# Kernel optimization log

Hardware: AMD Instinct MI355X
Metric: run time of the kernel (lower is better)

The kernel has to match this reference:

```python
import jax, jax.numpy as jnp
import numpy as np

V, D, H, B, S, K = 10000, 128, 512, 32, 512, 2  # vocab, emb, hidden, batch, seq, num_cells

def setup_inputs() -> dict:
    key = jax.random.key(0)
    ks = jax.random.split(key, 8)
    sc_d, sc_h = 1.0 / np.sqrt(D), 1.0 / np.sqrt(H)
    return {
        "x": jax.random.randint(ks[0], (B, S), 0, V),
        "emb_table": jax.random.normal(ks[1], (V, D), jnp.float32),
        "W_ih": jax.random.uniform(ks[2], (K, 4 * H, D), jnp.float32, -sc_d, sc_d),
        "W_hh": jax.random.uniform(ks[3], (K, 4 * H, H), jnp.float32, -sc_h, sc_h),
        "b_ih": jax.random.uniform(ks[4], (K, 4 * H), jnp.float32, -sc_h, sc_h),
        "b_hh": jax.random.uniform(ks[5], (K, 4 * H), jnp.float32, -sc_h, sc_h),
        "W_out": jax.random.uniform(ks[6], (V, H), jnp.float32, -sc_h, sc_h),
        "b_out": jax.random.uniform(ks[7], (V,), jnp.float32, -sc_h, sc_h),
    }

def _mlstm(x_ids_t, emb_t, W_ih, W_hh, b, h0, c0):
    # x_ids_t: (S,B) int, emb_t: (S,B,D). Two LSTMCells; token id parity picks the cell.
    def step(carry, inp):
        h, c = carry                       # (B,H) each
        xt, ids = inp                      # (B,D), (B,)
        gates = (jnp.einsum('bd,kgd->kbg', xt, W_ih)
                 + jnp.einsum('bh,kgh->kbg', h, W_hh)
                 + b[:, None, :])          # (K,B,4H)
        i, f, g, o = jnp.split(gates, 4, axis=-1)
        i, f, o = jax.nn.sigmoid(i), jax.nn.sigmoid(f), jax.nn.sigmoid(o)
        g = jnp.tanh(g)
        c_new = f * c + i * g              # (K,B,H)
        h_new = o * jnp.tanh(c_new)        # (K,B,H)
        sel = (ids % 2)[:, None]           # (B,1) cell index per example
        h_next = jnp.where(sel == 0, h_new[0], h_new[1])
        c_next = jnp.where(sel == 0, c_new[0], c_new[1])
        return (h_next, c_next), h_next
    (_, _), hs = jax.lax.scan(step, (h0, c0), (emb_t, x_ids_t))
    return hs  # (S,B,H)

def reference(x, emb_table, W_ih, W_hh, b_ih, b_hh, W_out, b_out):
    emb = emb_table[x]                     # (B,S,D)
    emb_t = jnp.transpose(emb, (1, 0, 2))  # (S,B,D) time-major
    h0 = jnp.zeros((x.shape[0], W_hh.shape[-1]), emb.dtype)
    hs = _mlstm(x.T, emb_t, W_ih, W_hh, b_ih + b_hh, h0, h0)  # (S,B,H)
    flat = hs.reshape(-1, hs.shape[-1])    # (S*B, H)
    logits = flat @ W_out.T + b_out        # (S*B, V)
    return jax.nn.log_softmax(logits, axis=1)
```

## Files before the change

### kernel.cpp

```cpp
#include <hip/hip_runtime.h>
#include <hip/hip_bf16.h>

typedef __attribute__((ext_vector_type(8))) short short8;
typedef __attribute__((ext_vector_type(4))) float f32x4;
typedef unsigned long long u64;

#define V_N 10000
#define D_E 128
#define H_N 512
#define B_N 32
#define S_N 512

#define SENT64 0xFFFFFFFFFFFFFFFFull

#define OFF_RP    0
#define OFF_EMB   5242880
#define OFF_HS    (OFF_EMB + 4194304)
#define OFF_WOUT  (OFF_HS + 16777216)

__device__ __forceinline__ float ftanh(float x) {
  float e = __expf(-2.f * fabsf(x));
  float r = (1.f - e) / (1.f + e);
  return __builtin_copysignf(r, x);
}

union U128 { f32x4 f; u64 q[2]; };

__global__ void k_prep_emb(const int* __restrict__ x, const float* __restrict__ tab,
                           __hip_bfloat16* __restrict__ emb) {
  int i = blockIdx.x * 256 + threadIdx.x;
  if (i >= S_N * B_N * D_E) return;
  int d  = i & (D_E - 1);
  int sb = i >> 7;
  int b  = sb & (B_N - 1);
  int s  = sb >> 5;
  int tok = x[b * S_N + s];
  emb[i] = __float2bfloat16(tab[tok * D_E + d]);
}

__global__ void k_prep_wout(const float* __restrict__ w, __hip_bfloat16* __restrict__ o) {
  int i = blockIdx.x * 256 + threadIdx.x;
  if (i < V_N * H_N) o[i] = __float2bfloat16(w[i]);
}

__launch_bounds__(256, 1)
__global__ void k_recurrence(const int* __restrict__ x,
                             const float* __restrict__ W_ih, const float* __restrict__ W_hh,
                             const float* __restrict__ b_ih, const float* __restrict__ b_hh,
                             const __hip_bfloat16* __restrict__ emb,
                             __hip_bfloat16* __restrict__ hs)
{
  __shared__ __align__(16) __hip_bfloat16 Bl[32][648];
  __shared__ float gl4[4][64][33];
  __shared__ float bias[64];
  __shared__ unsigned short hloc[8][32];

  const int tid = threadIdx.x;
  const int wg  = blockIdx.x;
  const int lane = tid & 63, kw = tid >> 6;
  const int lrow = lane & 15, lk = (lane >> 4) * 8;
  const int b_ep = tid & 31, jj_ep = tid >> 5;

  short8 Afrag[20];
  #pragma unroll
  for (int mt = 0; mt < 4; ++mt) {
    #pragma unroll
    for (int ks = 0; ks < 5; ++ks) {
      int lr = mt * 16 + lrow;
      int q = lr >> 4, kc = (lr >> 3) & 1, jj = lr & 7;
      int grow = kc * 2048 + q * 512 + wg * 8 + jj;
      int c0 = kw * 160 + ks * 32 + lk;
      short8 a;
      #pragma unroll
      for (int e = 0; e < 8; ++e) {
        int c = c0 + e;
        float v = (c < 128) ? W_ih[(size_t)grow * 128 + c]
                            : W_hh[(size_t)grow * 512 + (c - 128)];
        __hip_bfloat16 hb = __float2bfloat16(v);
        a[e] = *(const short*)&hb;
      }
      Afrag[mt * 5 + ks] = a;
    }
  }
  if (tid < 64) {
    int lr = tid;
    int q = lr >> 4, kc = (lr >> 3) & 1, jj = lr & 7;
    int grow = kc * 2048 + q * 512 + wg * 8 + jj;
    bias[lr] = b_ih[grow] + b_hh[grow];
  }

  unsigned par[16];
  #pragma unroll
  for (int w = 0; w < 16; ++w) {
    unsigned p = 0;
    for (int bb = 0; bb < 32; ++bb)
      p |= (unsigned)(x[b_ep * S_N + w * 32 + bb] & 1) << bb;
    par[w] = p;
  }

  float c_state = 0.f;

  for (int t = 0; t < S_N; ++t) {
    {
      const f32x4* e16 = (const f32x4*)(emb + (size_t)t * B_N * D_E);
      #pragma unroll
      for (int c = 0; c < 2; ++c) {
        int ci = c * 256 + tid;
        int ex = ci >> 4, col = ci & 15;
        *(f32x4*)((char*)&Bl[0][0] + ex * 1296 + col * 16) = e16[ci];
      }
    }
    if (t == 0) {
      for (int i = tid; i < 4096; i += 256) {
        int b = i >> 7, hh = i & 127;
        *(u64*)&Bl[b][128 + hh * 4] = 0ull;
      }
    } else {
      const char* srcb = (const char*)hs + (size_t)(t - 1) * 32768;
      U128 buf[8];
      unsigned pend = 0xFFu;
      while (pend) {
        #pragma unroll
        for (int c = 0; c < 8; ++c)
          if (pend & (1u << c))
            asm volatile("global_load_dwordx4 %0, %1, off sc0 sc1"
                         : "=v"(buf[c].f) : "v"(srcb + (c * 4096 + tid * 16)) : "memory");
        asm volatile("s_waitcnt vmcnt(0)" ::: "memory");
        __builtin_amdgcn_sched_barrier(0);
        #pragma unroll
        for (int c = 0; c < 8; ++c)
          if ((pend & (1u << c)) && buf[c].q[0] != SENT64 && buf[c].q[1] != SENT64) {
            int ci = c * 256 + tid;
            *(f32x4*)((char*)&Bl[0][0] + (ci >> 6) * 1296 + 256 + (ci & 63) * 16) = buf[c].f;
            pend &= ~(1u << c);
          }
      }
    }
    __syncthreads();

    {
      f32x4 acc[4][2] = {};
      #pragma unroll
      for (int ks = 0; ks < 5; ++ks) {
        int cb = (kw * 160 + ks * 32 + lk) * 2;
        short8 b0 = *(const short8*)((const char*)&Bl[0][0] + lrow * 1296 + cb);
        short8 b1 = *(const short8*)((const char*)&Bl[0][0] + (16 + lrow) * 1296 + cb);
        #pragma unroll
        for (int mt = 0; mt < 4; ++mt) {
          acc[mt][0] = __builtin_amdgcn_mfma_f32_16x16x32_bf16(Afrag[mt * 5 + ks], b0, acc[mt][0], 0, 0, 0);
          acc[mt][1] = __builtin_amdgcn_mfma_f32_16x16x32_bf16(Afrag[mt * 5 + ks], b1, acc[mt][1], 0, 0, 0);
        }
      }
      #pragma unroll
      for (int mt = 0; mt < 4; ++mt)
        #pragma unroll
        for (int nt = 0; nt < 2; ++nt)
          #pragma unroll
          for (int r = 0; r < 4; ++r)
            gl4[kw][mt * 16 + (lane >> 4) * 4 + r][nt * 16 + (lane & 15)] = acc[mt][nt][r];
    }
    __syncthreads();

    {
      float cand_c[2], cand_h[2];
      #pragma unroll
      for (int k = 0; k < 2; ++k) {
        int base = k * 8 + jj_ep;
        float ig = gl4[0][base][b_ep] + gl4[1][base][b_ep]
                 + gl4[2][base][b_ep] + gl4[3][base][b_ep] + bias[base];
        float fg = gl4[0][16 + base][b_ep] + gl4[1][16 + base][b_ep]
                 + gl4[2][16 + base][b_ep] + gl4[3][16 + base][b_ep] + bias[16 + base];
        float gg = gl4[0][32 + base][b_ep] + gl4[1][32 + base][b_ep]
                 + gl4[2][32 + base][b_ep] + gl4[3][32 + base][b_ep] + bias[32 + base];
        float og = gl4[0][48 + base][b_ep] + gl4[1][48 + base][b_ep]
                 + gl4[2][48 + base][b_ep] + gl4[3][48 + base][b_ep] + bias[48 + base];
        ig = 1.f / (1.f + __expf(-ig));
        fg = 1.f / (1.f + __expf(-fg));
        og = 1.f / (1.f + __expf(-og));
        gg = ftanh(gg);
        float cn = fg * c_state + ig * gg;
        cand_c[k] = cn;
        cand_h[k] = og * ftanh(cn);
      }
      int sel = (par[t >> 5] >> (t & 31)) & 1;
      c_state  = sel ? cand_c[1] : cand_c[0];
      float hv = sel ? cand_h[1] : cand_h[0];
      __hip_bfloat16 hb = __float2bfloat16(hv);
      hloc[jj_ep][b_ep] = *(const unsigned short*)&hb;
    }
    __syncthreads();

    if (tid < 64) {
      int b = tid >> 1, half = tid & 1;
      u64 v = (u64)hloc[half * 4 + 0][b]
            | ((u64)hloc[half * 4 + 1][b] << 16)
            | ((u64)hloc[half * 4 + 2][b] << 32)
            | ((u64)hloc[half * 4 + 3][b] << 48);
      u64* dst = (u64*)hs + (size_t)t * 4096 + b * 128 + wg * 2 + half;
      __hip_atomic_store(dst, v, __ATOMIC_RELAXED, __HIP_MEMORY_SCOPE_AGENT);
    }
  }
}

__launch_bounds__(256, 2)
__global__ void k_gemm(const __hip_bfloat16* __restrict__ hs,
                       const __hip_bfloat16* __restrict__ wout,
                       const float* __restrict__ b_out,
                       float* __restrict__ out,
                       float* __restrict__ rowpart)
{
  __shared__ __hip_bfloat16 Al[128][72];
  __shared__ __hip_bfloat16 Wt[128][72];
  __shared__ float sumLDS[2][128];
  const int tid = threadIdx.x;
  const int tn = blockIdx.x, tm = blockIdx.y;
  const int lane = tid & 63, wv = tid >> 6;
  const int mq = wv & 1, nq = wv >> 1;
  const int lrow = lane & 15, lk = (lane >> 4) * 8;
  f32x4 acc[4][4] = {};

  const int ar = tid >> 3, ac = (tid & 7) * 8;
  for (int k0 = 0; k0 < 512; k0 += 64) {
    __syncthreads();
    #pragma unroll
    for (int rr = 0; rr < 4; ++rr) {
      int r = ar + rr * 32;
      short8 av = *(const short8*)(hs + ((size_t)(tm * 128 + r)) * 512 + k0 + ac);
      *(short8*)&Al[r][ac] = av;
      int v = tn * 128 + r;
      short8 wvv = {};
      if (v < V_N) wvv = *(const short8*)(wout + (size_t)v * 512 + k0 + ac);
      *(short8*)&Wt[r][ac] = wvv;
    }
    __syncthreads();
    #pragma unroll
    for (int ks = 0; ks < 2; ++ks) {
      int kb = ks * 32 + lk;
      short8 af[4], bf[4];
      #pragma unroll
      for (int i = 0; i < 4; ++i) af[i] = *(const short8*)&Al[mq * 64 + i * 16 + lrow][kb];
      #pragma unroll
      for (int i = 0; i < 4; ++i) bf[i] = *(const short8*)&Wt[nq * 64 + i * 16 + lrow][kb];
      #pragma unroll
      for (int i = 0; i < 4; ++i)
        #pragma unroll
        for (int jx = 0; jx < 4; ++jx)
          acc[i][jx] = __builtin_amdgcn_mfma_f32_16x16x32_bf16(af[i], bf[jx], acc[i][jx], 0, 0, 0);
    }
  }
  const int rbase = tm * 128 + mq * 64 + (lane >> 4) * 4;
  const int cbase = tn * 128 + nq * 64 + (lane & 15);
  float esum[4][4];
  #pragma unroll
  for (int i = 0; i < 4; ++i)
    #pragma unroll
    for (int r = 0; r < 4; ++r) esum[i][r] = 0.f;

  #pragma unroll
  for (int i = 0; i < 4; ++i) {
    #pragma unroll
    for (int jx = 0; jx < 4; ++jx) {
      int col = cbase + jx * 16;
      if (col < V_N) {
        float bo = b_out[col];
        #pragma unroll
        for (int r = 0; r < 4; ++r) {
          int row = rbase + i * 16 + r;
          float lg = acc[i][jx][r] + bo;
          out[(size_t)row * V_N + col] = lg;
          esum[i][r] += __expf(lg);
        }
      }
    }
  }
  #pragma unroll
  for (int i = 0; i < 4; ++i) {
    #pragma unroll
    for (int r = 0; r < 4; ++r) {
      float s = esum[i][r];
      s += __shfl_xor(s, 1); s += __shfl_xor(s, 2);
      s += __shfl_xor(s, 4); s += __shfl_xor(s, 8);
      if ((lane & 15) == 0)
        sumLDS[nq][mq * 64 + i * 16 + (lane >> 4) * 4 + r] = s;
    }
  }
  __syncthreads();
  if (tid < 128)
    rowpart[(size_t)(tm * 128 + tid) * 80 + tn] = sumLDS[0][tid] + sumLDS[1][tid];
}

__launch_bounds__(256)
__global__ void k_lsm_fix(float* __restrict__ out, const float* __restrict__ rowpart) {
  const int r = blockIdx.x;
  const float* rp = rowpart + (size_t)r * 80;
  float s = 0.f;
  for (int p = 0; p < 79; ++p) s += rp[p];
  float lse = __logf(s);
  float4* q4 = (float4*)(out + (size_t)r * V_N);
  for (int i = threadIdx.x; i < V_N / 4; i += 256) {
    float4 v = q4[i];
    v.x -= lse; v.y -= lse; v.z -= lse; v.w -= lse;
    q4[i] = v;
  }
}

extern "C" void kernel_launch(void* const* d_in, const int* in_sizes, int n_in,
                              void* d_out, int out_size, void* d_ws, size_t ws_size,
                              hipStream_t stream) {
  const int*   x    = (const int*)d_in[0];
  const float* tab  = (const float*)d_in[1];
  const float* Wih  = (const float*)d_in[2];
  const float* Whh  = (const float*)d_in[3];
  const float* bih  = (const float*)d_in[4];
  const float* bhh  = (const float*)d_in[5];
  const float* Wout = (const float*)d_in[6];
  const float* bout = (const float*)d_in[7];
  float* out = (float*)d_out;

  char* ws = (char*)d_ws;
  float*           rowpart = (float*)(ws + OFF_RP);
  __hip_bfloat16*  emb     = (__hip_bfloat16*)(ws + OFF_EMB);
  __hip_bfloat16*  hsbuf   = (__hip_bfloat16*)(ws + OFF_HS);
  __hip_bfloat16*  wob     = (__hip_bfloat16*)(ws + OFF_WOUT);

  hipMemsetAsync(hsbuf, 0xFF, (size_t)S_N * B_N * H_N * 2, stream);
  k_prep_emb<<<(S_N * B_N * D_E) / 256, 256, 0, stream>>>(x, tab, emb);
  k_prep_wout<<<(V_N * H_N) / 256, 256, 0, stream>>>(Wout, wob);
  k_recurrence<<<64, 256, 0, stream>>>(x, Wih, Whh, bih, bhh, emb, hsbuf);
  k_gemm<<<dim3(79, 128), 256, 0, stream>>>(hsbuf, wob, bout, out, rowpart);
  k_lsm_fix<<<16384, 256, 0, stream>>>(out, rowpart);
}
```

Baseline: 2.556 ms.

## Repartition LSTM recurrence into 16 workgroups of 1024 threads

Measured after the change: 4.535 ms. 1.77x slower.

```diff
diff --git a/kernel.cpp b/kernel.cpp
--- a/kernel.cpp
+++ b/kernel.cpp
@@ -43,7 +43,7 @@
   if (i < V_N * H_N) o[i] = __float2bfloat16(w[i]);
 }
 
-__launch_bounds__(256, 1)
+__launch_bounds__(1024, 1)
 __global__ void k_recurrence(const int* __restrict__ x,
                              const float* __restrict__ W_ih, const float* __restrict__ W_hh,
                              const float* __restrict__ b_ih, const float* __restrict__ b_hh,
@@ -51,25 +51,26 @@
                              __hip_bfloat16* __restrict__ hs)
 {
   __shared__ __align__(16) __hip_bfloat16 Bl[32][648];
-  __shared__ float gl4[4][64][33];
-  __shared__ float bias[64];
-  __shared__ unsigned short hloc[8][32];
+  __shared__ float gl[2][256][33];
+  __shared__ float bias[256];
+  __shared__ unsigned short hloc[32][32];
 
   const int tid = threadIdx.x;
   const int wg  = blockIdx.x;
-  const int lane = tid & 63, kw = tid >> 6;
+  const int lane = tid & 63, wv = tid >> 6;
+  const int rg  = wv >> 1, ks2 = wv & 1;
   const int lrow = lane & 15, lk = (lane >> 4) * 8;
   const int b_ep = tid & 31, jj_ep = tid >> 5;
 
   short8 Afrag[20];
   #pragma unroll
-  for (int mt = 0; mt < 4; ++mt) {
-    #pragma unroll
-    for (int ks = 0; ks < 5; ++ks) {
-      int lr = mt * 16 + lrow;
-      int q = lr >> 4, kc = (lr >> 3) & 1, jj = lr & 7;
-      int grow = kc * 2048 + q * 512 + wg * 8 + jj;
-      int c0 = kw * 160 + ks * 32 + lk;
+  for (int mt = 0; mt < 2; ++mt) {
+    #pragma unroll
+    for (int ks = 0; ks < 10; ++ks) {
+      int lr = rg * 32 + mt * 16 + lrow;
+      int q = lr >> 6, kc = (lr >> 5) & 1, jj = lr & 31;
+      int grow = kc * 2048 + q * 512 + wg * 32 + jj;
+      int c0 = ks2 * 320 + ks * 32 + lk;
       short8 a;
       #pragma unroll
       for (int e = 0; e < 8; ++e) {
@@ -79,13 +80,13 @@
         __hip_bfloat16 hb = __float2bfloat16(v);
         a[e] = *(const short*)&hb;
       }
-      Afrag[mt * 5 + ks] = a;
-    }
-  }
-  if (tid < 64) {
+      Afrag[mt * 10 + ks] = a;
+    }
+  }
+  if (tid < 256) {
     int lr = tid;
-    int q = lr >> 4, kc = (lr >> 3) & 1, jj = lr & 7;
-    int grow = kc * 2048 + q * 512 + wg * 8 + jj;
+    int q = lr >> 6, kc = (lr >> 5) & 1, jj = lr & 31;
+    int grow = kc * 2048 + q * 512 + wg * 32 + jj;
     bias[lr] = b_ih[grow] + b_hh[grow];
   }
 
@@ -101,36 +102,32 @@
   float c_state = 0.f;
 
   for (int t = 0; t < S_N; ++t) {
-    {
+    if (tid < 512) {
       const f32x4* e16 = (const f32x4*)(emb + (size_t)t * B_N * D_E);
-      #pragma unroll
-      for (int c = 0; c < 2; ++c) {
-        int ci = c * 256 + tid;
-        int ex = ci >> 4, col = ci & 15;
-        *(f32x4*)((char*)&Bl[0][0] + ex * 1296 + col * 16) = e16[ci];
-      }
+      int ex = tid >> 4, col = tid & 15;
+      *(f32x4*)((char*)&Bl[0][0] + ex * 1296 + col * 16) = e16[tid];
     }
     if (t == 0) {
-      for (int i = tid; i < 4096; i += 256) {
+      for (int i = tid; i < 4096; i += 1024) {
         int b = i >> 7, hh = i & 127;
         *(u64*)&Bl[b][128 + hh * 4] = 0ull;
       }
     } else {
       const char* srcb = (const char*)hs + (size_t)(t - 1) * 32768;
-      U128 buf[8];
-      unsigned pend = 0xFFu;
+      U128 buf[2];
+      unsigned pend = 3u;
       while (pend) {
         #pragma unroll
-        for (int c = 0; c < 8; ++c)
+        for (int c = 0; c < 2; ++c)
           if (pend & (1u << c))
             asm volatile("global_load_dwordx4 %0, %1, off sc0 sc1"
-                         : "=v"(buf[c].f) : "v"(srcb + (c * 4096 + tid * 16)) : "memory");
+                         : "=v"(buf[c].f) : "v"(srcb + (c * 16384 + tid * 16)) : "memory");
         asm volatile("s_waitcnt vmcnt(0)" ::: "memory");
         __builtin_amdgcn_sched_barrier(0);
         #pragma unroll
-        for (int c = 0; c < 8; ++c)
+        for (int c = 0; c < 2; ++c)
           if ((pend & (1u << c)) && buf[c].q[0] != SENT64 && buf[c].q[1] != SENT64) {
-            int ci = c * 256 + tid;
+            int ci = c * 1024 + tid;
             *(f32x4*)((char*)&Bl[0][0] + (ci >> 6) * 1296 + 256 + (ci & 63) * 16) = buf[c].f;
             pend &= ~(1u << c);
           }
@@ -139,48 +136,44 @@
     __syncthreads();
 
     {
-      f32x4 acc[4][2] = {};
-      #pragma unroll
-      for (int ks = 0; ks < 5; ++ks) {
-        int cb = (kw * 160 + ks * 32 + lk) * 2;
+      f32x4 acc[2][2] = {};
+      #pragma unroll
+      for (int ks = 0; ks < 10; ++ks) {
+        int cb = (ks2 * 320 + ks * 32 + lk) * 2;
         short8 b0 = *(const short8*)((const char*)&Bl[0][0] + lrow * 1296 + cb);
         short8 b1 = *(const short8*)((const char*)&Bl[0][0] + (16 + lrow) * 1296 + cb);
         #pragma unroll
-        for (int mt = 0; mt < 4; ++mt) {
-          acc[mt][0] = __builtin_amdgcn_mfma_f32_16x16x32_bf16(Afrag[mt * 5 + ks], b0, acc[mt][0], 0, 0, 0);
-          acc[mt][1] = __builtin_amdgcn_mfma_f32_16x16x32_bf16(Afrag[mt * 5 + ks], b1, acc[mt][1], 0, 0, 0);
+        for (int mt = 0; mt < 2; ++mt) {
+          acc[mt][0] = __builtin_amdgcn_mfma_f32_16x16x32_bf16(Afrag[mt * 10 + ks], b0, acc[mt][0], 0, 0, 0);
+          acc[mt][1] = __builtin_amdgcn_mfma_f32_16x16x32_bf16(Afrag[mt * 10 + ks], b1, acc[mt][1], 0, 0, 0);
         }
       }
       #pragma unroll
-      for (int mt = 0; mt < 4; ++mt)
+      for (int mt = 0; mt < 2; ++mt)
         #pragma unroll
         for (int nt = 0; nt < 2; ++nt)
           #pragma unroll
           for (int r = 0; r < 4; ++r)
-            gl4[kw][mt * 16 + (lane >> 4) * 4 + r][nt * 16 + (lane & 15)] = acc[mt][nt][r];
+            gl[ks2][rg * 32 + mt * 16 + (lane >> 4) * 4 + r][nt * 16 + (lane & 15)] = acc[mt][nt][r];
     }
     __syncthreads();
 
     {
       float cand_c[2], cand_h[2];
       #pragma unroll
-      for (int k = 0; k < 2; ++k) {
-        int base = k * 8 + jj_ep;
-        float ig = gl4[0][base][b_ep] + gl4[1][base][b_ep]
-                 + gl4[2][base][b_ep] + gl4[3][base][b_ep] + bias[base];
-        float fg = gl4[0][16 + base][b_ep] + gl4[1][16 + base][b_ep]
-                 + gl4[2][16 + base][b_ep] + gl4[3][16 + base][b_ep] + bias[16 + base];
-        float gg = gl4[0][32 + base][b_ep] + gl4[1][32 + base][b_ep]
-                 + gl4[2][32 + base][b_ep] + gl4[3][32 + base][b_ep] + bias[32 + base];
-        float og = gl4[0][48 + base][b_ep] + gl4[1][48 + base][b_ep]
-                 + gl4[2][48 + base][b_ep] + gl4[3][48 + base][b_ep] + bias[48 + base];
+      for (int kc = 0; kc < 2; ++kc) {
+        int base = kc * 32 + jj_ep;
+        float ig = gl[0][base][b_ep]       + gl[1][base][b_ep]       + bias[base];
+        float fg = gl[0][64 + base][b_ep]  + gl[1][64 + base][b_ep]  + bias[64 + base];
+        float gg = gl[0][128 + base][b_ep] + gl[1][128 + base][b_ep] + bias[128 + base];
+        float og = gl[0][192 + base][b_ep] + gl[1][192 + base][b_ep] + bias[192 + base];
         ig = 1.f / (1.f + __expf(-ig));
         fg = 1.f / (1.f + __expf(-fg));
         og = 1.f / (1.f + __expf(-og));
         gg = ftanh(gg);
         float cn = fg * c_state + ig * gg;
-        cand_c[k] = cn;
-        cand_h[k] = og * ftanh(cn);
+        cand_c[kc] = cn;
+        cand_h[kc] = og * ftanh(cn);
       }
       int sel = (par[t >> 5] >> (t & 31)) & 1;
       c_state  = sel ? cand_c[1] : cand_c[0];
@@ -190,13 +183,13 @@
     }
     __syncthreads();
 
-    if (tid < 64) {
-      int b = tid >> 1, half = tid & 1;
-      u64 v = (u64)hloc[half * 4 + 0][b]
-            | ((u64)hloc[half * 4 + 1][b] << 16)
-            | ((u64)hloc[half * 4 + 2][b] << 32)
-            | ((u64)hloc[half * 4 + 3][b] << 48);
-      u64* dst = (u64*)hs + (size_t)t * 4096 + b * 128 + wg * 2 + half;
+    if (tid < 256) {
+      int ex = tid >> 3, part = tid & 7;
+      u64 v = (u64)hloc[part * 4 + 0][ex]
+            | ((u64)hloc[part * 4 + 1][ex] << 16)
+            | ((u64)hloc[part * 4 + 2][ex] << 32)
+            | ((u64)hloc[part * 4 + 3][ex] << 48);
+      u64* dst = (u64*)hs + (size_t)t * 4096 + ex * 128 + wg * 8 + part;
       __hip_atomic_store(dst, v, __ATOMIC_RELAXED, __HIP_MEMORY_SCOPE_AGENT);
     }
   }
@@ -326,7 +319,7 @@
   hipMemsetAsync(hsbuf, 0xFF, (size_t)S_N * B_N * H_N * 2, stream);
   k_prep_emb<<<(S_N * B_N * D_E) / 256, 256, 0, stream>>>(x, tab, emb);
   k_prep_wout<<<(V_N * H_N) / 256, 256, 0, stream>>>(Wout, wob);
-  k_recurrence<<<64, 256, 0, stream>>>(x, Wih, Whh, bih, bhh, emb, hsbuf);
+  k_recurrence<<<16, 1024, 0, stream>>>(x, Wih, Whh, bih, bhh, emb, hsbuf);
   k_gemm<<<dim3(79, 128), 256, 0, stream>>>(hsbuf, wob, bout, out, rowpart);
   k_lsm_fix<<<16384, 256, 0, stream>>>(out, rowpart);
 }
```
